# Kernel optimization log

Measured on AMD Instinct MI355X. Metric: run time of the kernel, lower is better.

The kernel has to match this reference:

```python
import jax, jax.numpy as jnp
import numpy as np

T, B, S = 12, 65536, 1024       # time steps, total pedestrians, scenes
P = B // S                      # peds per scene (uniform segments)
H_DIM = 64                      # enc_h_dim
D = 4 * H_DIM                   # 256 = concat(h_fwd,h_rev,c_fwd,c_rev)
MLP = 32                        # mlp_dim (obs_enc_feat width)
ZS = 32                         # zS_dim


def setup_inputs() -> dict:
    key = jax.random.key(0)
    ks = jax.random.split(key, 16)
    sc = 1.0 / np.sqrt(H_DIM)
    G = 4 * H_DIM  # gate width (i,f,g,o)
    starts = jnp.arange(S, dtype=jnp.int32) * P
    seq_start_end = jnp.stack([starts, starts + P], axis=1)
    return {
        "last_obs_traj": jax.random.normal(ks[0], (B, 6), jnp.float32),
        "fut_rel_traj": jax.random.normal(ks[1], (T, B, 2), jnp.float32),
        "seq_start_end": seq_start_end,
        "obs_enc_feat": jax.random.normal(ks[2], (B, MLP), jnp.float32),
        "fut_obst": jnp.zeros((T, S, 1), jnp.float32),  # unused by forward
        # initial_h_model / initial_c_model (Linear 6 -> H_DIM)
        "w_h0": jax.random.normal(ks[3], (6, H_DIM), jnp.float32) * sc,
        "b_h0": jnp.zeros((H_DIM,), jnp.float32),
        "w_c0": jax.random.normal(ks[4], (6, H_DIM), jnp.float32) * sc,
        "b_c0": jnp.zeros((H_DIM,), jnp.float32),
        # bidirectional LSTM (input 2, hidden H_DIM), gate order i,f,g,o
        "w_ih_f": jax.random.normal(ks[5], (2, G), jnp.float32) * sc,
        "w_hh_f": jax.random.normal(ks[6], (H_DIM, G), jnp.float32) * sc,
        "b_f": jnp.zeros((G,), jnp.float32),
        "w_ih_r": jax.random.normal(ks[7], (2, G), jnp.float32) * sc,
        "w_hh_r": jax.random.normal(ks[8], (H_DIM, G), jnp.float32) * sc,
        "b_r": jnp.zeros((G,), jnp.float32),
        # fc2: Linear(4h + 4h + mlp_dim -> zS_dim)
        "w_fc2": jax.random.normal(ks[9], (2 * D + MLP, ZS), jnp.float32) * 0.05,
        "b_fc2": jnp.zeros((ZS,), jnp.float32),
    }


def _lstm_scan(xs, h0, c0, w_ih, w_hh, b):
    """Run an LSTM over xs (T,B,in); return final (h, c). Gate order i,f,g,o."""
    def step(carry, x):
        h, c = carry
        z = x @ w_ih + h @ w_hh + b
        i, f, g, o = jnp.split(z, 4, axis=-1)
        c = jax.nn.sigmoid(f) * c + jax.nn.sigmoid(i) * jnp.tanh(g)
        h = jax.nn.sigmoid(o) * jnp.tanh(c)
        return (h, c), None
    (hT, cT), _ = jax.lax.scan(step, (h0, c0), xs)
    return hT, cT


def reference(last_obs_traj, fut_rel_traj, seq_start_end, obs_enc_feat, fut_obst,
              w_h0, b_h0, w_c0, b_c0,
              w_ih_f, w_hh_f, b_f, w_ih_r, w_hh_r, b_r,
              w_fc2, b_fc2):
    # initial states: forward direction from linear maps, reverse direction zeros
    h0_f = last_obs_traj @ w_h0 + b_h0
    c0_f = last_obs_traj @ w_c0 + b_c0
    zeros = jnp.zeros_like(h0_f)

    hf, cf = _lstm_scan(fut_rel_traj, h0_f, c0_f, w_ih_f, w_hh_f, b_f)
    hr, cr = _lstm_scan(fut_rel_traj[::-1], zeros, zeros, w_ih_r, w_hh_r, b_r)

    # torch: state = cat((h_n, c_n), dim=0).permute(1,0,2).reshape(B, 4h)
    final_encoder_h = jnp.concatenate([hf, hr, cf, cr], axis=1)  # (B, 256)

    # per-scene softmax attention pooling: context = softmax(H H^T) @ H
    n_scenes = seq_start_end.shape[0]
    Hs = final_encoder_h.reshape(n_scenes, -1, final_encoder_h.shape[1])  # (S,P,D)
    attn = jax.nn.softmax(jnp.einsum('spd,sqd->spq', Hs, Hs), axis=-1)
    pool_h = jnp.einsum('spq,sqd->spd', attn, Hs).reshape(final_encoder_h.shape)

    dist_fc_input = jnp.concatenate([final_encoder_h, pool_h, obs_enc_feat], axis=1)
    stats = dist_fc_input @ w_fc2 + b_fc2
    return dist_fc_input, stats
```

## Files before the change

kernel.cpp:

```cpp
#include <hip/hip_runtime.h>

#define T_STEPS 12
#define NPED 65536
#define NSCENE 1024
#define PSC 64
#define HID 64
#define DDIM 256
#define DIST 544
#define ZS 32

typedef unsigned int u32;
typedef unsigned short u16;
typedef __attribute__((ext_vector_type(8))) short bf16x8;
typedef __attribute__((ext_vector_type(4))) float f32x4;

__device__ __forceinline__ float u2f(u32 u) { union { u32 i; float f; } v; v.i = u; return v.f; }
__device__ __forceinline__ u32 f2u(float f) { union { float f; u32 i; } v; v.f = f; return v.i; }
__device__ __forceinline__ float bf2f(u16 u) { return u2f(((u32)u) << 16); }
__device__ __forceinline__ u16 f2bf(float f) {
  u32 i = f2u(f);
  return (u16)((i + 0x7fffu + ((i >> 16) & 1u)) >> 16);
}
__device__ __forceinline__ u32 pack2(float a, float b) { return (u32)f2bf(a) | (((u32)f2bf(b)) << 16); }

__device__ __forceinline__ float fsig(float x) { return __builtin_amdgcn_rcpf(1.0f + __expf(-x)); }
__device__ __forceinline__ float ftanh(float x) {
  float e = __expf(fminf(fmaxf(2.0f * x, -80.0f), 80.0f));
  return (e - 1.0f) * __builtin_amdgcn_rcpf(e + 1.0f);
}
__device__ __forceinline__ void unpack8(const uint4 v, float* f) {
  f[0] = u2f(v.x << 16); f[1] = u2f(v.x & 0xffff0000u);
  f[2] = u2f(v.y << 16); f[3] = u2f(v.y & 0xffff0000u);
  f[4] = u2f(v.z << 16); f[5] = u2f(v.z & 0xffff0000u);
  f[6] = u2f(v.w << 16); f[7] = u2f(v.w & 0xffff0000u);
}

__device__ __forceinline__ bool inputs_are_bf16(const u16* probe) {
  const int lane = threadIdx.x & 63;
  const u16 w = probe[2 * lane];
  const u32 e = (w >> 7) & 0xffu;
  const bool ok = (w == 0) || (e >= 96u && e <= 144u);
  return __popcll(__ballot(ok)) >= 48;
}

template<bool FP32>
__device__ __forceinline__ float ld(const void* p, int idx) {
  if (FP32) return ((const float*)p)[idx];
  return bf2f(((const u16*)p)[idx]);
}
template<bool FP32>
__device__ __forceinline__ void ld8(const void* p, size_t idx8, float* f) {
  if (FP32) {
    const float4 a = ((const float4*)p)[idx8 >> 2];
    const float4 b = ((const float4*)p)[(idx8 >> 2) + 1];
    f[0] = a.x; f[1] = a.y; f[2] = a.z; f[3] = a.w;
    f[4] = b.x; f[5] = b.y; f[6] = b.z; f[7] = b.w;
  } else {
    unpack8(((const uint4*)p)[idx8 >> 3], f);
  }
}
template<bool FP32>
__device__ __forceinline__ void ldpair(const void* p, size_t pairidx, float& a, float& b) {
  if (FP32) {
    const float2 v = ((const float2*)p)[pairidx];
    a = v.x; b = v.y;
  } else {
    const u32 xx = ((const u32*)p)[pairidx];
    a = u2f(xx << 16); b = u2f(xx & 0xffff0000u);
  }
}
template<bool FP32>
__device__ __forceinline__ void st8(void* p, size_t idx8, const float* f) {
  if (FP32) {
    float4 a; a.x = f[0]; a.y = f[1]; a.z = f[2]; a.w = f[3];
    float4 b; b.x = f[4]; b.y = f[5]; b.z = f[6]; b.w = f[7];
    ((float4*)p)[idx8 >> 2] = a;
    ((float4*)p)[(idx8 >> 2) + 1] = b;
  } else {
    uint4 pk;
    pk.x = pack2(f[0], f[1]); pk.y = pack2(f[2], f[3]);
    pk.z = pack2(f[4], f[5]); pk.w = pack2(f[6], f[7]);
    ((uint4*)p)[idx8 >> 3] = pk;
  }
}
template<bool FP32>
__device__ __forceinline__ void st4(void* p, size_t idx4, const float4 v) {
  if (FP32) {
    ((float4*)p)[idx4 >> 2] = v;
  } else {
    uint2 pk; pk.x = pack2(v.x, v.y); pk.y = pack2(v.z, v.w);
    *(uint2*)((u16*)p + idx4) = pk;
  }
}

template<bool FP32>
__device__ __forceinline__ void lstm_body(
    const void* __restrict__ last_obs, const void* __restrict__ fut,
    const void* __restrict__ w_h0, const void* __restrict__ b_h0,
    const void* __restrict__ w_c0, const void* __restrict__ b_c0,
    const void* __restrict__ w_ih_f, const void* __restrict__ w_hh_f, const void* __restrict__ b_gf,
    const void* __restrict__ w_ih_r, const void* __restrict__ w_hh_r, const void* __restrict__ b_gr,
    void* __restrict__ outv,
    u16* __restrict__ wTp, u16* __restrict__ wXp, u16* __restrict__ hbp)
{
  const int tid  = threadIdx.x;
  const int wave = tid >> 6;
  const int lane = tid & 63;
  const int l15  = lane & 15;
  const int lhi  = lane >> 4;
  const int ped0 = blockIdx.x * 64 + wave * 16;
  const int xm   = (lane & 7) << 4;
  const int e0   = (lhi * 16) ^ xm;
  const int e1   = (64 + lhi * 16) ^ xm;
  const int foff0 = l15 * 128 + e0;
  const int foff1 = l15 * 128 + e1;
  char* const hw = (char*)hbp + wave * 2048;
  char* const wb = (char*)wTp;
  char* const wxrow = (char*)wXp + l15 * 128;

  float c[16];

  for (int dir = 0; dir < 2; ++dir) {
    const void* whh = dir ? w_hh_r : w_hh_f;
    const void* wih = dir ? w_ih_r : w_ih_f;
    const void* bg  = dir ? b_gr  : b_gf;

    __syncthreads();
    #pragma unroll
    for (int c8 = 0; c8 < 8; ++c8) {
      const int n = tid, k0 = c8 * 8;
      u32 pk[4];
      #pragma unroll
      for (int h = 0; h < 4; ++h) {
        u16 ea, eb;
        if (FP32) {
          ea = f2bf(((const float*)whh)[(k0 + 2 * h) * DDIM + n]);
          eb = f2bf(((const float*)whh)[(k0 + 2 * h + 1) * DDIM + n]);
        } else {
          ea = ((const u16*)whh)[(k0 + 2 * h) * DDIM + n];
          eb = ((const u16*)whh)[(k0 + 2 * h + 1) * DDIM + n];
        }
        pk[h] = (u32)ea | ((u32)eb << 16);
      }
      uint4 v; v.x = pk[0]; v.y = pk[1]; v.z = pk[2]; v.w = pk[3];
      *(uint4*)(wb + n * 128 + ((k0 * 2) ^ ((n & 7) << 4))) = v;
    }
    {
      const int tg2 = tid >> 4, col = tid & 15;
      const float wi0 = ld<FP32>(wih, tg2 * 16 + col);
      const float wi1 = ld<FP32>(wih, DDIM + tg2 * 16 + col);
      const float bb  = ld<FP32>(bg,  tg2 * 16 + col);
      char* const wx = (char*)wXp;
      const int base = (tg2 >> 1) * 2048 + col * 128;
      const int kofs = (tg2 & 1) * 64;
      const int swz  = (col & 7) << 4;
      uint4 v0; v0.x = pack2(wi0, wi1); v0.y = (u32)f2bf(bb); v0.z = 0u; v0.w = 0u;
      uint4 zz; zz.x = 0u; zz.y = 0u; zz.z = 0u; zz.w = 0u;
      *(uint4*)(wx + base + ((kofs +  0) ^ swz)) = v0;
      *(uint4*)(wx + base + ((kofs + 16) ^ swz)) = zz;
      *(uint4*)(wx + base + ((kofs + 32) ^ swz)) = zz;
      *(uint4*)(wx + base + ((kofs + 48) ^ swz)) = zz;
    }

    if (dir == 0) {
      float xo[4][6];
      #pragma unroll
      for (int r = 0; r < 4; ++r)
        #pragma unroll
        for (int k = 0; k < 6; ++k)
          xo[r][k] = ld<FP32>(last_obs, (ped0 + lhi * 4 + r) * 6 + k);
      #pragma unroll
      for (int jj = 0; jj < 4; ++jj) {
        const int j = jj * 16 + l15;
        float wh[6], wc[6];
        #pragma unroll
        for (int k = 0; k < 6; ++k) {
          wh[k] = ld<FP32>(w_h0, k * HID + j);
          wc[k] = ld<FP32>(w_c0, k * HID + j);
        }
        const float bh = ld<FP32>(b_h0, j), bc = ld<FP32>(b_c0, j);
        #pragma unroll
        for (int r = 0; r < 4; ++r) {
          float h0 = bh, c0 = bc;
          #pragma unroll
          for (int k = 0; k < 6; ++k) {
            h0 = fmaf(xo[r][k], wh[k], h0);
            c0 = fmaf(xo[r][k], wc[k], c0);
          }
          c[jj * 4 + r] = c0;
          const int p = lhi * 4 + r;
          *(u16*)(hw + p * 128 + ((j * 2) ^ ((p & 7) << 4))) = f2bf(h0);
        }
      }
    } else {
      #pragma unroll
      for (int jj = 0; jj < 4; ++jj) {
        const int j = jj * 16 + l15;
        #pragma unroll
        for (int r = 0; r < 4; ++r) {
          c[jj * 4 + r] = 0.0f;
          const int p = lhi * 4 + r;
          *(u16*)(hw + p * 128 + ((j * 2) ^ ((p & 7) << 4))) = 0;
        }
      }
    }
    __syncthreads();

    for (int t = 0; t < T_STEPS; ++t) {
      const int tt = dir ? (T_STEPS - 1 - t) : t;
      float xa, xb2;
      ldpair<FP32>(fut, (size_t)tt * NPED + ped0 + l15, xa, xb2);
      union { bf16x8 v; u32 w[4]; } ax;
      ax.w[0] = (lhi == 0) ? pack2(xa, xb2) : 0u;
      ax.w[1] = (lhi == 0) ? 0x00003f80u : 0u;
      ax.w[2] = 0u; ax.w[3] = 0u;

      __asm__ volatile("" ::: "memory");
      const bf16x8 a0 = *(const bf16x8*)(hw + foff0);
      const bf16x8 a1 = *(const bf16x8*)(hw + foff1);

      f32x4 acc[16];
      #pragma unroll
      for (int tg = 0; tg < 16; ++tg) {
        const bf16x8 bx = *(const bf16x8*)(wxrow + (tg >> 1) * 2048 + ((tg & 1) ? e1 : e0));
        const bf16x8 b0 = *(const bf16x8*)(wb + tg * 2048 + foff0);
        const bf16x8 b1 = *(const bf16x8*)(wb + tg * 2048 + foff1);
        f32x4 z = {0.0f, 0.0f, 0.0f, 0.0f};
        z = __builtin_amdgcn_mfma_f32_16x16x32_bf16(ax.v, bx, z, 0, 0, 0);
        z = __builtin_amdgcn_mfma_f32_16x16x32_bf16(a0, b0, z, 0, 0, 0);
        acc[tg] = __builtin_amdgcn_mfma_f32_16x16x32_bf16(a1, b1, z, 0, 0, 0);
      }
      __asm__ volatile("" ::: "memory");

      #pragma unroll
      for (int jj = 0; jj < 4; ++jj) {
        const int j = jj * 16 + l15;
        #pragma unroll
        for (int r = 0; r < 4; ++r) {
          const float ig = fsig(acc[jj][r]);
          const float fg = fsig(acc[jj + 4][r]);
          const float gg = ftanh(acc[jj + 8][r]);
          const float og = fsig(acc[jj + 12][r]);
          const float cn = fmaf(fg, c[jj * 4 + r], ig * gg);
          c[jj * 4 + r] = cn;
          const float hn = og * ftanh(cn);
          const int p = lhi * 4 + r;
          *(u16*)(hw + p * 128 + ((j * 2) ^ ((p & 7) << 4))) = f2bf(hn);
        }
      }
      __asm__ volatile("" ::: "memory");
    }

    __syncthreads();
    float* const tb = (float*)wTp + wave * 1024;
    #pragma unroll
    for (int jj = 0; jj < 4; ++jj)
      #pragma unroll
      for (int r = 0; r < 4; ++r)
        tb[(lhi * 4 + r) * 64 + jj * 16 + l15] = c[jj * 4 + r];
    __asm__ volatile("" ::: "memory");
    #pragma unroll
    for (int r = 0; r < 4; ++r) {
      const int pl = r * 4 + lhi;
      const u32* hp = (const u32*)(hw + pl * 128 + ((l15 * 8) ^ ((pl & 7) << 4)));
      const u32 h01 = hp[0], h23 = hp[1];
      float4 hv;
      hv.x = u2f(h01 << 16); hv.y = u2f(h01 & 0xffff0000u);
      hv.z = u2f(h23 << 16); hv.w = u2f(h23 & 0xffff0000u);
      const float4 cv = *(const float4*)&tb[pl * 64 + l15 * 4];
      const size_t rb = (size_t)(ped0 + pl) * DIST;
      st4<FP32>(outv, rb + (dir ? 64 : 0) + l15 * 4, hv);
      st4<FP32>(outv, rb + 128 + (dir ? 64 : 0) + l15 * 4, cv);
    }
  }
}

__global__ __launch_bounds__(256, 2)
void lstm_kernel(const void* last_obs, const void* fut,
                 const void* w_h0, const void* b_h0,
                 const void* w_c0, const void* b_c0,
                 const void* w_ih_f, const void* w_hh_f, const void* b_gf,
                 const void* w_ih_r, const void* w_hh_r, const void* b_gr,
                 void* outv)
{
  __shared__ __align__(16) u16 wT[DDIM * HID];
  __shared__ __align__(16) u16 wX[8 * 1024];
  __shared__ __align__(16) u16 hb[4][16 * HID];
  if (inputs_are_bf16((const u16*)fut))
    lstm_body<false>(last_obs, fut, w_h0, b_h0, w_c0, b_c0,
                     w_ih_f, w_hh_f, b_gf, w_ih_r, w_hh_r, b_gr, outv, wT, wX, &hb[0][0]);
  else
    lstm_body<true>(last_obs, fut, w_h0, b_h0, w_c0, b_c0,
                    w_ih_f, w_hh_f, b_gf, w_ih_r, w_hh_r, b_gr, outv, wT, wX, &hb[0][0]);
}

template<bool FP32>
__device__ __forceinline__ void pool_body(
    const void* __restrict__ obs, const void* __restrict__ wfc,
    const void* __restrict__ bfc, void* __restrict__ outv,
    u16* __restrict__ Hrow, u16* __restrict__ Breg)
{
  const int tid  = threadIdx.x;
  const int wave = tid >> 6;
  const int lane = tid & 63;
  const int l15  = lane & 15;
  const int lhi  = lane >> 4;
  const int pedbase = blockIdx.x * PSC;
  const int wbase = wave * 16;
  char* const hb = (char*)Hrow;
  char* const tr = (char*)Breg;
  char* const pb = (char*)Breg + 32768;
  const int swl = (l15 & 7) << 4;

  if (FP32) {
    const float* ob = (const float*)outv;
    for (int i = tid; i < PSC * 64; i += 256) {
      const int pp = i >> 6, dd = (i & 63) << 2;
      const float4 v = *(const float4*)(ob + (size_t)(pedbase + pp) * DIST + dd);
      uint2 w; w.x = pack2(v.x, v.y); w.y = pack2(v.z, v.w);
      *(uint2*)(hb + pp * 512 + ((2 * dd) ^ ((pp & 7) << 4))) = w;
    }
  } else {
    const u16* ob = (const u16*)outv;
    for (int i = tid; i < PSC * 32; i += 256) {
      const int pp = i >> 5, dd = (i & 31) << 3;
      *(uint4*)(hb + pp * 512 + ((2 * dd) ^ ((pp & 7) << 4))) =
          *(const uint4*)(ob + (size_t)(pedbase + pp) * DIST + dd);
    }
  }
  __syncthreads();

  {
    const int p = tid >> 2, q4 = tid & 3;
    const int swp = (p & 7) << 4;
    #pragma unroll
    for (int j = 0; j < 8; ++j) {
      const int d0 = q4 * 64 + j * 8;
      const uint4 v = *(const uint4*)(hb + p * 512 + ((2 * d0) ^ swp));
      const u16* e = (const u16*)&v;
      #pragma unroll
      for (int jj = 0; jj < 8; ++jj) {
        const int d = d0 + jj;
        *(u16*)(tr + d * 128 + ((2 * p) ^ ((d & 7) << 4))) = e[jj];
      }
    }
  }

  f32x4 acc[4];
  #pragma unroll
  for (int b = 0; b < 4; ++b) acc[b] = (f32x4){0.0f, 0.0f, 0.0f, 0.0f};
  for (int kt = 0; kt < 8; ++kt) {
    const int ko = kt * 64 + lhi * 16;
    const bf16x8 af = *(const bf16x8*)(hb + (wbase + l15) * 512 + (ko ^ swl));
    #pragma unroll
    for (int b = 0; b < 4; ++b) {
      const bf16x8 bf = *(const bf16x8*)(hb + (b * 16 + l15) * 512 + (ko ^ swl));
      acc[b] = __builtin_amdgcn_mfma_f32_16x16x32_bf16(af, bf, acc[b], 0, 0, 0);
    }
  }

  float P[4][4];
  #pragma unroll
  for (int r = 0; r < 4; ++r) {
    float mx = fmaxf(fmaxf(acc[0][r], acc[1][r]), fmaxf(acc[2][r], acc[3][r]));
    mx = fmaxf(mx, __shfl_xor(mx, 1));
    mx = fmaxf(mx, __shfl_xor(mx, 2));
    mx = fmaxf(mx, __shfl_xor(mx, 4));
    mx = fmaxf(mx, __shfl_xor(mx, 8));
    float s = 0.0f;
    #pragma unroll
    for (int b = 0; b < 4; ++b) { P[b][r] = __expf(acc[b][r] - mx); s += P[b][r]; }
    s += __shfl_xor(s, 1); s += __shfl_xor(s, 2);
    s += __shfl_xor(s, 4); s += __shfl_xor(s, 8);
    const float inv = __builtin_amdgcn_rcpf(s);
    #pragma unroll
    for (int b = 0; b < 4; ++b) P[b][r] *= inv;
  }

  #pragma unroll
  for (int b = 0; b < 4; ++b)
    #pragma unroll
    for (int r = 0; r < 4; ++r) {
      const int p = wbase + lhi * 4 + r, q = b * 16 + l15;
      *(u16*)(pb + p * 128 + ((2 * q) ^ ((p & 7) << 4))) = f2bf(P[b][r]);
    }
  __syncthreads();

  float* const stg = (float*)(hb + wave * 8192);
  const bf16x8 pa0 = *(const bf16x8*)(pb + (wbase + l15) * 128 + ((     lhi * 16) ^ swl));
  const bf16x8 pa1 = *(const bf16x8*)(pb + (wbase + l15) * 128 + ((64 + lhi * 16) ^ swl));
  for (int Q = 0; Q < 4; ++Q) {
    f32x4 pv[4];
    #pragma unroll
    for (int n = 0; n < 4; ++n) {
      const int d = (Q * 4 + n) * 16 + l15;
      const int swd = (d & 7) << 4;
      const bf16x8 b0 = *(const bf16x8*)(tr + d * 128 + ((     lhi * 16) ^ swd));
      const bf16x8 b1 = *(const bf16x8*)(tr + d * 128 + ((64 + lhi * 16) ^ swd));
      f32x4 z = {0.0f, 0.0f, 0.0f, 0.0f};
      z = __builtin_amdgcn_mfma_f32_16x16x32_bf16(pa0, b0, z, 0, 0, 0);
      pv[n] = __builtin_amdgcn_mfma_f32_16x16x32_bf16(pa1, b1, z, 0, 0, 0);
    }
    __asm__ volatile("" ::: "memory");
    #pragma unroll
    for (int n = 0; n < 4; ++n)
      #pragma unroll
      for (int r = 0; r < 4; ++r)
        stg[(lhi * 4 + r) * 64 + n * 16 + l15] = pv[n][r];
    __asm__ volatile("" ::: "memory");
    #pragma unroll
    for (int r = 0; r < 4; ++r) {
      const int pl = r * 4 + lhi;
      const float4 cv = *(const float4*)&stg[pl * 64 + l15 * 4];
      st4<FP32>(outv, (size_t)(pedbase + wbase + pl) * DIST + DDIM + Q * 64 + l15 * 4, cv);
    }
    __asm__ volatile("" ::: "memory");
  }

  {
    const int p = tid >> 2, part = tid & 3;
    float ov[8];
    ld8<FP32>(obs, (size_t)(pedbase + p) * ZS + part * 8, ov);
    st8<FP32>(outv, (size_t)(pedbase + p) * DIST + 2 * DDIM + part * 8, ov);
  }

  __syncthreads();

  for (int i = tid; i < DIST * ZS; i += 256) {
    const int k = i >> 5, z = i & 31;
    const u16 w = FP32 ? f2bf(((const float*)wfc)[i]) : ((const u16*)wfc)[i];
    *(u16*)(tr + (k >> 5) * 2048 + z * 64 + ((2 * (k & 31)) ^ ((z & 3) << 4))) = w;
  }
  __syncthreads();

  {
    const size_t rowb = (size_t)(pedbase + wbase + l15) * DIST;
    f32x4 s0 = {0.0f, 0.0f, 0.0f, 0.0f}, s1 = {0.0f, 0.0f, 0.0f, 0.0f};
    const int bofs = (lhi * 16) ^ ((l15 & 3) << 4);
    for (int kt = 0; kt < 17; ++kt) {
      const int kd = kt * 32 + lhi * 8;
      union { bf16x8 v; uint4 u; } af;
      if (FP32) {
        const float4 a = *(const float4*)((const float*)outv + rowb + kd);
        const float4 b = *(const float4*)((const float*)outv + rowb + kd + 4);
        af.u.x = pack2(a.x, a.y); af.u.y = pack2(a.z, a.w);
        af.u.z = pack2(b.x, b.y); af.u.w = pack2(b.z, b.w);
      } else {
        af.u = *(const uint4*)((const u16*)outv + rowb + kd);
      }
      const char* wfb = tr + kt * 2048;
      const bf16x8 b0 = *(const bf16x8*)(wfb + (l15     ) * 64 + bofs);
      const bf16x8 b1 = *(const bf16x8*)(wfb + (l15 + 16) * 64 + bofs);
      s0 = __builtin_amdgcn_mfma_f32_16x16x32_bf16(af.v, b0, s0, 0, 0, 0);
      s1 = __builtin_amdgcn_mfma_f32_16x16x32_bf16(af.v, b1, s1, 0, 0, 0);
    }
    const float bb0 = ld<FP32>(bfc, l15), bb1 = ld<FP32>(bfc, 16 + l15);
    __asm__ volatile("" ::: "memory");
    #pragma unroll
    for (int r = 0; r < 4; ++r) {
      stg[(lhi * 4 + r) * 32 + l15     ] = s0[r] + bb0;
      stg[(lhi * 4 + r) * 32 + l15 + 16] = s1[r] + bb1;
    }
    __asm__ volatile("" ::: "memory");
    #pragma unroll
    for (int s = 0; s < 2; ++s) {
      const int idx = lane * 2 + s;
      const int pl = idx >> 3, q4 = idx & 7;
      const float4 v = *(const float4*)&stg[pl * 32 + q4 * 4];
      st4<FP32>(outv, (size_t)NPED * DIST + (size_t)(pedbase + wbase + pl) * ZS + q4 * 4, v);
    }
  }
}

__global__ __launch_bounds__(256, 2)
void pool_kernel(const void* fut, const void* obs, const void* wfc,
                 const void* bfc, void* outv)
{
  __shared__ __align__(16) u16 Hrow[PSC * DDIM];
  __shared__ __align__(16) u16 Breg[20480];
  if (inputs_are_bf16((const u16*)fut)) pool_body<false>(obs, wfc, bfc, outv, Hrow, Breg);
  else                                  pool_body<true>(obs, wfc, bfc, outv, Hrow, Breg);
}

extern "C" void kernel_launch(void* const* d_in, const int* in_sizes, int n_in,
                              void* d_out, int out_size, void* d_ws, size_t ws_size,
                              hipStream_t stream) {
  const void* last_obs = d_in[0];
  const void* fut      = d_in[1];
  const void* obs      = d_in[3];
  const void* w_h0  = d_in[5];
  const void* b_h0  = d_in[6];
  const void* w_c0  = d_in[7];
  const void* b_c0  = d_in[8];
  const void* w_ih_f = d_in[9];
  const void* w_hh_f = d_in[10];
  const void* b_f    = d_in[11];
  const void* w_ih_r = d_in[12];
  const void* w_hh_r = d_in[13];
  const void* b_r    = d_in[14];
  const void* w_fc2  = d_in[15];
  const void* b_fc2  = d_in[16];

  lstm_kernel<<<dim3(NPED / 64), dim3(256), 0, stream>>>(
      last_obs, fut, w_h0, b_h0, w_c0, b_c0,
      w_ih_f, w_hh_f, b_f, w_ih_r, w_hh_r, b_r, d_out);
  pool_kernel<<<dim3(NSCENE), dim3(256), 0, stream>>>(fut, obs, w_fc2, b_fc2, d_out);
}
```

Before: 402.5 us.

## Feed fc2 GEMM from registers and LDS instead of re-reading output from global

Before, the fc2 stage re-read each pedestrian's 544-wide concatenated row from global memory, which the same kernel had just written. Now the encoder part comes from the LDS H tile, the pooled context is converted to bf16 fragments in registers as it is produced, and the obs features are loaded directly into a fragment. This removes a large global read-after-write per block. In exchange it adds register pressure (8 extra bf16x8 fragments), reshapes the PV staging into 32-column chunks in the P buffer, and fully unrolls the k loop.

```diff
diff --git a/kernel.cpp b/kernel.cpp
--- a/kernel.cpp
+++ b/kernel.cpp
@@ -386,14 +386,16 @@
     }
   __syncthreads();
 
-  float* const stg = (float*)(hb + wave * 8192);
   const bf16x8 pa0 = *(const bf16x8*)(pb + (wbase + l15) * 128 + ((     lhi * 16) ^ swl));
   const bf16x8 pa1 = *(const bf16x8*)(pb + (wbase + l15) * 128 + ((64 + lhi * 16) ^ swl));
-  for (int Q = 0; Q < 4; ++Q) {
-    f32x4 pv[4];
-    #pragma unroll
-    for (int n = 0; n < 4; ++n) {
-      const int d = (Q * 4 + n) * 16 + l15;
+  float* const stgp = (float*)(pb + wave * 2048);
+  bf16x8 pf[8];
+  #pragma unroll
+  for (int e = 0; e < 8; ++e) {
+    f32x4 pv[2];
+    #pragma unroll
+    for (int n = 0; n < 2; ++n) {
+      const int d = e * 32 + n * 16 + l15;
       const int swd = (d & 7) << 4;
       const bf16x8 b0 = *(const bf16x8*)(tr + d * 128 + ((     lhi * 16) ^ swd));
       const bf16x8 b1 = *(const bf16x8*)(tr + d * 128 + ((64 + lhi * 16) ^ swd));
@@ -403,25 +405,41 @@
     }
     __asm__ volatile("" ::: "memory");
     #pragma unroll
-    for (int n = 0; n < 4; ++n)
+    for (int n = 0; n < 2; ++n)
       #pragma unroll
       for (int r = 0; r < 4; ++r)
-        stg[(lhi * 4 + r) * 64 + n * 16 + l15] = pv[n][r];
+        stgp[(lhi * 4 + r) * 32 + n * 16 + l15] = pv[n][r];
     __asm__ volatile("" ::: "memory");
     #pragma unroll
-    for (int r = 0; r < 4; ++r) {
-      const int pl = r * 4 + lhi;
-      const float4 cv = *(const float4*)&stg[pl * 64 + l15 * 4];
-      st4<FP32>(outv, (size_t)(pedbase + wbase + pl) * DIST + DDIM + Q * 64 + l15 * 4, cv);
+    for (int s = 0; s < 2; ++s) {
+      const int idx = lane * 2 + s;
+      const int pl = idx >> 3, q = idx & 7;
+      const float4 v = *(const float4*)&stgp[pl * 32 + q * 4];
+      st4<FP32>(outv, (size_t)(pedbase + wbase + pl) * DIST + DDIM + e * 32 + q * 4, v);
+    }
+    {
+      const float4 a = *(const float4*)&stgp[l15 * 32 + lhi * 8];
+      const float4 b = *(const float4*)&stgp[l15 * 32 + lhi * 8 + 4];
+      union { bf16x8 v; uint4 u; } fr;
+      fr.u.x = pack2(a.x, a.y); fr.u.y = pack2(a.z, a.w);
+      fr.u.z = pack2(b.x, b.y); fr.u.w = pack2(b.z, b.w);
+      pf[e] = fr.v;
     }
     __asm__ volatile("" ::: "memory");
   }
 
+  bf16x8 of;
   {
     const int p = tid >> 2, part = tid & 3;
     float ov[8];
     ld8<FP32>(obs, (size_t)(pedbase + p) * ZS + part * 8, ov);
     st8<FP32>(outv, (size_t)(pedbase + p) * DIST + 2 * DDIM + part * 8, ov);
+    float om[8];
+    ld8<FP32>(obs, (size_t)(pedbase + wbase + l15) * ZS + lhi * 8, om);
+    union { bf16x8 v; uint4 u; } fr;
+    fr.u.x = pack2(om[0], om[1]); fr.u.y = pack2(om[2], om[3]);
+    fr.u.z = pack2(om[4], om[5]); fr.u.w = pack2(om[6], om[7]);
+    of = fr.v;
   }
 
   __syncthreads();
@@ -434,40 +452,40 @@
   __syncthreads();
 
   {
-    const size_t rowb = (size_t)(pedbase + wbase + l15) * DIST;
     f32x4 s0 = {0.0f, 0.0f, 0.0f, 0.0f}, s1 = {0.0f, 0.0f, 0.0f, 0.0f};
     const int bofs = (lhi * 16) ^ ((l15 & 3) << 4);
+    #pragma unroll
     for (int kt = 0; kt < 17; ++kt) {
-      const int kd = kt * 32 + lhi * 8;
-      union { bf16x8 v; uint4 u; } af;
-      if (FP32) {
-        const float4 a = *(const float4*)((const float*)outv + rowb + kd);
-        const float4 b = *(const float4*)((const float*)outv + rowb + kd + 4);
-        af.u.x = pack2(a.x, a.y); af.u.y = pack2(a.z, a.w);
-        af.u.z = pack2(b.x, b.y); af.u.w = pack2(b.z, b.w);
+      bf16x8 av;
+      if (kt < 8) {
+        const int ko = kt * 64 + lhi * 16;
+        av = *(const bf16x8*)(hb + (wbase + l15) * 512 + (ko ^ swl));
+      } else if (kt < 16) {
+        av = pf[kt - 8];
       } else {
-        af.u = *(const uint4*)((const u16*)outv + rowb + kd);
+        av = of;
       }
       const char* wfb = tr + kt * 2048;
       const bf16x8 b0 = *(const bf16x8*)(wfb + (l15     ) * 64 + bofs);
       const bf16x8 b1 = *(const bf16x8*)(wfb + (l15 + 16) * 64 + bofs);
-      s0 = __builtin_amdgcn_mfma_f32_16x16x32_bf16(af.v, b0, s0, 0, 0, 0);
-      s1 = __builtin_amdgcn_mfma_f32_16x16x32_bf16(af.v, b1, s1, 0, 0, 0);
+      s0 = __builtin_amdgcn_mfma_f32_16x16x32_bf16(av, b0, s0, 0, 0, 0);
+      s1 = __builtin_amdgcn_mfma_f32_16x16x32_bf16(av, b1, s1, 0, 0, 0);
     }
     const float bb0 = ld<FP32>(bfc, l15), bb1 = ld<FP32>(bfc, 16 + l15);
+    float* const stgh = (float*)(hb + wave * 8192);
     __asm__ volatile("" ::: "memory");
     #pragma unroll
     for (int r = 0; r < 4; ++r) {
-      stg[(lhi * 4 + r) * 32 + l15     ] = s0[r] + bb0;
-      stg[(lhi * 4 + r) * 32 + l15 + 16] = s1[r] + bb1;
+      stgh[(lhi * 4 + r) * 32 + l15     ] = s0[r] + bb0;
+      stgh[(lhi * 4 + r) * 32 + l15 + 16] = s1[r] + bb1;
     }
     __asm__ volatile("" ::: "memory");
     #pragma unroll
     for (int s = 0; s < 2; ++s) {
       const int idx = lane * 2 + s;
-      const int pl = idx >> 3, q4 = idx & 7;
-      const float4 v = *(const float4*)&stg[pl * 32 + q4 * 4];
-      st4<FP32>(outv, (size_t)NPED * DIST + (size_t)(pedbase + wbase + pl) * ZS + q4 * 4, v);
+      const int pl = idx >> 3, q = idx & 7;
+      const float4 v = *(const float4*)&stgh[pl * 32 + q * 4];
+      st4<FP32>(outv, (size_t)NPED * DIST + (size_t)(pedbase + wbase + pl) * ZS + q * 4, v);
     }
   }
 }
```

Measured after the change: 387.4 us. 3.8% less time.
